# Kernel tuning notes

Measured on AMD Instinct MI355X. Metric: run time of the kernel, lower is better.

Reference implementation:

```python
import jax, jax.numpy as jnp
import numpy as np
import math

B, T, D, H, E, K = 2, 1024, 1024, 2048, 8, 2
CAP_FRAC = 0.25


def setup_inputs() -> dict:
    key = jax.random.key(0)
    ks = jax.random.split(key, 6)
    s = 0.02  # weight scale (orig uses TruncatedNormal; scale kept sane)
    return {
        "x": jax.random.normal(ks[0], (B, T, D), dtype=jnp.float32),
        "router_w": jax.random.normal(ks[1], (D, E), dtype=jnp.float32) * s,
        "router_b": jax.random.normal(ks[2], (E,), dtype=jnp.float32) * s,
        "w1": jax.random.normal(ks[3], (E, D, H), dtype=jnp.float32) * s,
        "w2": jax.random.normal(ks[4], (E, D, H), dtype=jnp.float32) * s,
        "w3": jax.random.normal(ks[5], (E, H, D), dtype=jnp.float32) * s,
    }


def reference(x, router_w, router_b, w1, w2, w3):
    b, t, d = x.shape
    Bt = b * t
    cap = math.floor(Bt * CAP_FRAC)  # expert capacity C (static)
    x_flat = x.reshape(Bt, d)

    # ---- router: fp32 scores, top-k, softmax over selected experts ----
    scores = x_flat.astype(jnp.float32) @ router_w + router_b  # (Bt, E)
    top_scores, assign = jax.lax.top_k(scores, K)               # (Bt, K)
    gates = jax.nn.softmax(top_scores, axis=-1).astype(x.dtype)

    # ---- capacity-based token->expert assignment via one-hot cumsum ----
    onehot = jax.nn.one_hot(assign, E)                          # (Bt, K, E)
    pos = jnp.cumsum(jnp.cumsum(onehot, axis=0), axis=1).astype(jnp.int32)
    mask = onehot * jnp.less(pos, cap)                          # (Bt, K, E)
    token_mask = jnp.sum(mask, axis=-1)                         # (Bt, K)
    # dispatch tensor: (E, C, Bt)
    choices = jnp.sum(jax.nn.one_hot(pos, cap) * mask[..., None], axis=1)
    choices = choices.transpose(1, 2, 0).astype(jnp.int32)
    e_id = jnp.einsum('tke,e->tk', mask, jnp.arange(E, dtype=mask.dtype)).astype(jnp.int32)
    p_id = jnp.einsum('tke,tke->tk', mask, pos.astype(mask.dtype)).astype(jnp.int32)

    # ---- dispatch ----
    grouped = jnp.einsum('ect,td->ecd', choices.astype(x.dtype), x_flat)  # (E, C, D)

    # ---- grouped expert FFN: gelu(w2(x) * w1(x)) @ w3 ----
    h = jnp.einsum('ecd,edh->ech', grouped, w2) * jnp.einsum('ecd,edh->ech', grouped, w1)
    h = jax.nn.gelu(h)
    eo = jnp.einsum('ech,ehd->ecd', h, w3)                      # (E, C, D)

    # ---- combine ----
    e_id = e_id.reshape(b, t, K)
    p_id = p_id.reshape(b, t, K)
    token_mask = token_mask.reshape(b, t, K)
    gates = gates.reshape(b, t, K)
    out = eo[e_id, p_id]                                        # (b, t, K, D)
    out = jnp.where(token_mask[..., None].astype(bool), out, x[..., None, :])
    return jnp.einsum('btkd,btk->btd', out, gates)
```

## Files before the change

kernel.cpp:

```cpp
#include <hip/hip_runtime.h>
#include <hip/hip_bf16.h>
#include <math.h>

#define BT   2048
#define DD   1024
#define HH   2048
#define EE   8
#define CAP  512

typedef unsigned short u16;
typedef unsigned int   u32;
typedef short bf16x8 __attribute__((ext_vector_type(8)));
typedef float f32x4  __attribute__((ext_vector_type(4)));
typedef u16   u16x4  __attribute__((ext_vector_type(4)));

#define AS1 __attribute__((address_space(1)))
#define AS3 __attribute__((address_space(3)))

__device__ __forceinline__ u16 f2bf(float f) {
    union { float f; u32 u; } v; v.f = f;
    return (u16)((v.u + 0x7fffu + ((v.u >> 16) & 1u)) >> 16);
}
__device__ __forceinline__ float bf2f(u16 b) {
    union { u32 u; float f; } v; v.u = ((u32)b) << 16;
    return v.f;
}
__device__ __forceinline__ u32 pkbf(float lo, float hi) {
    u32 r;
    asm("v_cvt_pk_bf16_f32 %0, %1, %2" : "=v"(r) : "v"(lo), "v"(hi));
    return r;
}

__global__ __launch_bounds__(256) void router_kernel(
    const float* __restrict__ x, const float* __restrict__ rw,
    const float* __restrict__ rb, int2* __restrict__ assign,
    float2* __restrict__ gates)
{
    int t   = blockIdx.x;
    int tid = threadIdx.x;
    const float* xr = x + (size_t)t * DD;

    float p[EE];
    #pragma unroll
    for (int e = 0; e < EE; ++e) p[e] = 0.f;

    for (int d = tid; d < DD; d += 256) {
        float xv = xr[d];
        const float4* wr = (const float4*)(rw + (size_t)d * EE);
        float4 w0 = wr[0], w1 = wr[1];
        p[0] += xv * w0.x; p[1] += xv * w0.y; p[2] += xv * w0.z; p[3] += xv * w0.w;
        p[4] += xv * w1.x; p[5] += xv * w1.y; p[6] += xv * w1.z; p[7] += xv * w1.w;
    }
    #pragma unroll
    for (int off = 32; off; off >>= 1) {
        #pragma unroll
        for (int e = 0; e < EE; ++e) p[e] += __shfl_down(p[e], off);
    }
    __shared__ float red[4][EE];
    int wv = tid >> 6, ln = tid & 63;
    if (ln == 0) {
        #pragma unroll
        for (int e = 0; e < EE; ++e) red[wv][e] = p[e];
    }
    __syncthreads();
    if (tid == 0) {
        float s[EE];
        #pragma unroll
        for (int e = 0; e < EE; ++e)
            s[e] = red[0][e] + red[1][e] + red[2][e] + red[3][e] + rb[e];
        int i0 = 0;
        #pragma unroll
        for (int e = 1; e < EE; ++e) if (s[e] > s[i0]) i0 = e;
        int i1 = -1;
        #pragma unroll
        for (int e = 0; e < EE; ++e) {
            if (e == i0) continue;
            if (i1 < 0 || s[e] > s[i1]) i1 = e;
        }
        float e1 = expf(s[i1] - s[i0]);
        float denom = 1.0f + e1;
        assign[t] = make_int2(i0, i1);
        gates[t]  = make_float2(1.0f / denom, e1 / denom);
    }
}

__global__ __launch_bounds__(64) void scan_kernel(
    const int2* __restrict__ assign, int4* __restrict__ meta,
    int2* __restrict__ slot_tok)
{
    __shared__ int c0[64][EE];
    __shared__ int cA[64][EE];
    int l = threadIdx.x;

    for (int i = l; i < EE * CAP; i += 64) slot_tok[i] = make_int2(-1, -1);
    #pragma unroll
    for (int e = 0; e < EE; ++e) { c0[l][e] = 0; cA[l][e] = 0; }
    __syncthreads();

    const int CH = BT / 64;
    int t0 = l * CH;

    for (int t = t0; t < t0 + CH; ++t) {
        int2 a = assign[t];
        c0[l][a.x]++; cA[l][a.x]++; cA[l][a.y]++;
    }
    __syncthreads();

    #pragma unroll
    for (int e = 0; e < EE; ++e) {
        int v = c0[l][e], inc = v;
        for (int d = 1; d < 64; d <<= 1) { int u = __shfl_up(inc, d); if (l >= d) inc += u; }
        c0[l][e] = inc - v;
        v = cA[l][e]; inc = v;
        for (int d = 1; d < 64; d <<= 1) { int u = __shfl_up(inc, d); if (l >= d) inc += u; }
        cA[l][e] = inc - v;
    }
    __syncthreads();

    for (int t = t0; t < t0 + CH; ++t) {
        int2 a = assign[t];
        int p0 = ++c0[l][a.x];  cA[l][a.x]++;
        int p1 = ++cA[l][a.y];
        int4 m;
        m.x = a.x; m.y = (p0 < CAP) ? p0 : -1;
        m.z = a.y; m.w = (p1 < CAP) ? p1 : -1;
        meta[t] = m;
        int* st = (int*)slot_tok;
        if (p0 < CAP) st[(a.x * CAP + p0) * 2 + 0] = t;
        if (p1 < CAP) st[(a.y * CAP + p1) * 2 + 1] = t;
    }
}

__global__ __launch_bounds__(256) void gather_bf16(
    const float* __restrict__ x, const int2* __restrict__ slot_tok,
    u16* __restrict__ G)
{
    int es = blockIdx.x;
    int d  = threadIdx.x * 4;
    int2 st = slot_tok[es];
    float4 r = make_float4(0.f, 0.f, 0.f, 0.f);
    if (st.x >= 0) r = *(const float4*)(x + (size_t)st.x * DD + d);
    if (st.y >= 0) {
        float4 v = *(const float4*)(x + (size_t)st.y * DD + d);
        r.x += v.x; r.y += v.y; r.z += v.z; r.w += v.w;
    }
    u16x4 o;
    o[0] = f2bf(r.x); o[1] = f2bf(r.y); o[2] = f2bf(r.z); o[3] = f2bf(r.w);
    *(u16x4*)(G + (size_t)es * DD + d) = o;
}


__global__ __launch_bounds__(256, 2) void gemm1_mfma(
    const u16* __restrict__ G, const float* __restrict__ W1,
    const float* __restrict__ W2, u16* __restrict__ H)
{
    __shared__ u16   As [128 * 64];
    __shared__ float B1s[64 * 64];
    __shared__ float B2s[64 * 64];

    const int bid  = blockIdx.x;
    const int e    = bid & 7;
    const int rest = bid >> 3;
    const int m0   = (rest & 3) * 128;
    const int n0   = (rest >> 2) * 64;

    const int tid  = threadIdx.x;
    const int lane = tid & 63;
    const int w    = tid >> 6;
    const int lr = lane & 15, lq = lane >> 4;

    const char* Ab  = (const char*)(G + (size_t)e * CAP * DD + (size_t)m0 * DD);
    const char* W1b = (const char*)(W1 + (size_t)e * DD * HH + n0);
    const char* W2b = (const char*)(W2 + (size_t)e * DD * HH + n0);

    const int srow = lane >> 2;
    const int skb  = ((lane & 3) ^ ((lane >> 3) & 3)) * 16;
    const int brow_i = lane >> 4;

    f32x4 acc1[8] = {};
    f32x4 acc2[8] = {};

    for (int k0 = 0; k0 < DD; k0 += 64) {
        #pragma unroll
        for (int j = 0; j < 4; ++j) {
            const int idx = 4 * w + j;
            const int h = idx >> 3, c = idx & 7;
            const size_t rb = (size_t)(c * 16 + srow) * (DD * 2)
                            + (size_t)k0 * 2 + h * 64 + skb;
            __builtin_amdgcn_global_load_lds((const AS1 void*)(Ab + rb),
                (AS3 void*)((char*)As + idx * 1024), 16, 0, 0);
        }
        #pragma unroll
        for (int i = 0; i < 4; ++i) {
            const int krow = w * 16 + i * 4 + brow_i;
            const int bscc = ((lane & 15) ^ ((5 * (2 * w + (i >> 1))) & 15)) * 16;
            const size_t sb = (size_t)(k0 + krow) * (HH * 4) + bscc;
            __builtin_amdgcn_global_load_lds((const AS1 void*)(W1b + sb),
                (AS3 void*)((char*)B1s + w * 4096 + i * 1024), 16, 0, 0);
            __builtin_amdgcn_global_load_lds((const AS1 void*)(W2b + sb),
                (AS3 void*)((char*)B2s + w * 4096 + i * 1024), 16, 0, 0);
        }
        __syncthreads();
        #pragma unroll
        for (int h = 0; h < 2; ++h) {
            bf16x8 av[8];
            #pragma unroll
            for (int m = 0; m < 8; ++m) {
                const int row = m * 16 + lr;
                const int sl  = (lq ^ ((row >> 1) & 3)) * 16;
                av[m] = *(const bf16x8*)((const char*)As + h * 8192 + row * 64 + sl);
            }
            const int n   = w * 16 + lr;
            const int lqh = h * 4 + lq;
            const int cb  = ((((n >> 2) ^ (5 * lqh)) & 15) << 4) + (n & 3) * 4;
            union { u32 q[4]; bf16x8 v; } u1, u2;
            #pragma unroll
            for (int i = 0; i < 4; ++i) {
                int o = (lqh * 8 + 2 * i) * 256 + cb;
                asm("" : "+v"(o));
                u1.q[i] = pkbf(*(const float*)((const char*)B1s + o),
                               *(const float*)((const char*)B1s + o + 256));
                u2.q[i] = pkbf(*(const float*)((const char*)B2s + o),
                               *(const float*)((const char*)B2s + o + 256));
            }
            const bf16x8 b1 = u1.v, b2 = u2.v;
            #pragma unroll
            for (int m = 0; m < 8; ++m) {
                acc1[m] = __builtin_amdgcn_mfma_f32_16x16x32_bf16(av[m], b1, acc1[m], 0, 0, 0);
                acc2[m] = __builtin_amdgcn_mfma_f32_16x16x32_bf16(av[m], b2, acc2[m], 0, 0, 0);
            }
        }
        __syncthreads();
    }

    u16* He = H + (size_t)e * CAP * HH;
    const float gc0 = 0.7978845608028654f, gc1 = 0.044715f;
    const int cc = n0 + w * 16 + lr;
    #pragma unroll
    for (int m = 0; m < 8; ++m)
        #pragma unroll
        for (int r = 0; r < 4; ++r) {
            const int rr = m0 + m * 16 + lq * 4 + r;
            float hv = acc1[m][r] * acc2[m][r];
            float u  = gc0 * (hv + gc1 * hv * hv * hv);
            float th = 1.f - 2.f / (__expf(2.f * u) + 1.f);
            He[(size_t)rr * HH + cc] = f2bf(0.5f * hv * (1.f + th));
        }
}

__global__ __launch_bounds__(256, 2) void gemm2_mfma(
    const u16* __restrict__ Hin, const float* __restrict__ W3, u16* __restrict__ EO)
{
    __shared__ u16   As[128 * 64];
    __shared__ float Bs[64 * 64];

    const int bid  = blockIdx.x;
    const int e    = bid & 7;
    const int rest = bid >> 3;
    const int m0   = (rest & 3) * 128;
    const int n0   = (rest >> 2) * 64;

    const int tid  = threadIdx.x;
    const int lane = tid & 63;
    const int w    = tid >> 6;
    const int lr = lane & 15, lq = lane >> 4;

    const char* Ab  = (const char*)(Hin + (size_t)e * CAP * HH + (size_t)m0 * HH);
    const char* W3b = (const char*)(W3 + (size_t)e * HH * DD + n0);

    const int srow = lane >> 2;
    const int skb  = ((lane & 3) ^ ((lane >> 3) & 3)) * 16;
    const int brow_i = lane >> 4;

    f32x4 acc[8] = {};

    for (int k0 = 0; k0 < HH; k0 += 64) {
        #pragma unroll
        for (int j = 0; j < 4; ++j) {
            const int idx = 4 * w + j;
            const int h = idx >> 3, c = idx & 7;
            const size_t rb = (size_t)(c * 16 + srow) * (HH * 2)
                            + (size_t)k0 * 2 + h * 64 + skb;
            __builtin_amdgcn_global_load_lds((const AS1 void*)(Ab + rb),
                (AS3 void*)((char*)As + idx * 1024), 16, 0, 0);
        }
        #pragma unroll
        for (int i = 0; i < 4; ++i) {
            const int krow = w * 16 + i * 4 + brow_i;
            const int bscc = ((lane & 15) ^ ((5 * (2 * w + (i >> 1))) & 15)) * 16;
            const size_t sb = (size_t)(k0 + krow) * (DD * 4) + bscc;
            __builtin_amdgcn_global_load_lds((const AS1 void*)(W3b + sb),
                (AS3 void*)((char*)Bs + w * 4096 + i * 1024), 16, 0, 0);
        }
        __syncthreads();
        #pragma unroll
        for (int h = 0; h < 2; ++h) {
            bf16x8 av[8];
            #pragma unroll
            for (int m = 0; m < 8; ++m) {
                const int row = m * 16 + lr;
                const int sl  = (lq ^ ((row >> 1) & 3)) * 16;
                av[m] = *(const bf16x8*)((const char*)As + h * 8192 + row * 64 + sl);
            }
            const int n   = w * 16 + lr;
            const int lqh = h * 4 + lq;
            const int cb  = ((((n >> 2) ^ (5 * lqh)) & 15) << 4) + (n & 3) * 4;
            union { u32 q[4]; bf16x8 v; } u3;
            #pragma unroll
            for (int i = 0; i < 4; ++i) {
                int o = (lqh * 8 + 2 * i) * 256 + cb;
                asm("" : "+v"(o));
                u3.q[i] = pkbf(*(const float*)((const char*)Bs + o),
                               *(const float*)((const char*)Bs + o + 256));
            }
            const bf16x8 b3 = u3.v;
            #pragma unroll
            for (int m = 0; m < 8; ++m)
                acc[m] = __builtin_amdgcn_mfma_f32_16x16x32_bf16(av[m], b3, acc[m], 0, 0, 0);
        }
        __syncthreads();
    }

    u16* Oe = EO + (size_t)e * CAP * DD;
    const int cc = n0 + w * 16 + lr;
    #pragma unroll
    for (int m = 0; m < 8; ++m)
        #pragma unroll
        for (int r = 0; r < 4; ++r) {
            const int rr = m0 + m * 16 + lq * 4 + r;
            Oe[(size_t)rr * DD + cc] = f2bf(acc[m][r]);
        }
}

__global__ __launch_bounds__(256) void combine_kernel(
    const float* __restrict__ x, const u16* __restrict__ EO,
    const int4* __restrict__ meta, const float2* __restrict__ gates,
    float* __restrict__ out)
{
    int t = blockIdx.x;
    int d = threadIdx.x * 4;
    int4  m = meta[t];
    float2 g = gates[t];
    float4 xv = *(const float4*)(x + (size_t)t * DD + d);
    float4 v0 = xv, v1 = xv;
    if (m.y >= 0) {
        u16x4 q = *(const u16x4*)(EO + ((size_t)m.x * CAP + m.y) * DD + d);
        v0 = make_float4(bf2f(q[0]), bf2f(q[1]), bf2f(q[2]), bf2f(q[3]));
    }
    if (m.w >= 0) {
        u16x4 q = *(const u16x4*)(EO + ((size_t)m.z * CAP + m.w) * DD + d);
        v1 = make_float4(bf2f(q[0]), bf2f(q[1]), bf2f(q[2]), bf2f(q[3]));
    }
    float4 r;
    r.x = g.x * v0.x + g.y * v1.x;
    r.y = g.x * v0.y + g.y * v1.y;
    r.z = g.x * v0.z + g.y * v1.z;
    r.w = g.x * v0.w + g.y * v1.w;
    *(float4*)(out + (size_t)t * DD + d) = r;
}

extern "C" void kernel_launch(void* const* d_in, const int* in_sizes, int n_in,
                              void* d_out, int out_size, void* d_ws, size_t ws_size,
                              hipStream_t stream)
{
    const float* x  = (const float*)d_in[0];
    const float* rw = (const float*)d_in[1];
    const float* rb = (const float*)d_in[2];
    const float* w1 = (const float*)d_in[3];
    const float* w2 = (const float*)d_in[4];
    const float* w3 = (const float*)d_in[5];
    float* out = (float*)d_out;

    char* ws = (char*)d_ws;
    size_t off = 0;
    auto alloc = [&](size_t bytes) { char* p = ws + off; off = (off + bytes + 255) & ~(size_t)255; return p; };

    int2*   assign   = (int2*)  alloc(BT * sizeof(int2));
    float2* gates    = (float2*)alloc(BT * sizeof(float2));
    int4*   meta     = (int4*)  alloc(BT * sizeof(int4));
    int2*   slot_tok = (int2*)  alloc(EE * CAP * sizeof(int2));
    u16*    grouped  = (u16*)   alloc((size_t)EE * CAP * DD * 2);
    u16*    Hbuf     = (u16*)   alloc((size_t)EE * CAP * HH * 2);
    u16*    eo       = (u16*)   alloc((size_t)EE * CAP * DD * 2);
    (void)ws_size;

    router_kernel<<<BT, 256, 0, stream>>>(x, rw, rb, assign, gates);
    scan_kernel<<<1, 64, 0, stream>>>(assign, meta, slot_tok);
    gather_bf16<<<EE * CAP, 256, 0, stream>>>(x, slot_tok, grouped);

    gemm1_mfma<<<1024, 256, 0, stream>>>(grouped, w1, w2, Hbuf);
    gemm2_mfma<<<512, 256, 0, stream>>>(Hbuf, w3, eo);

    combine_kernel<<<BT, 256, 0, stream>>>(x, eo, meta, gates, out);
}
```

Measured before the change: 128.4 us.

## Split fused dual-weight GEMM1 into two single-weight GEMMs plus elementwise mul-GELU kernel

The fused gemm1 kernel, which computed both w1 and w2 projections and applied the mul-GELU epilogue, becomes a single-weight GEMM launched twice. Each launch writes fp32 results to new workspace buffers, and a separate elementwise kernel multiplies them, applies GELU and writes bf16. This lowers per-block register and LDS pressure, which may help occupancy. The cost is rereading the A tiles twice and a large fp32 round trip through global memory (two 32 MB writes plus reads), along with extra launches.

```diff
diff --git a/kernel.cpp b/kernel.cpp
--- a/kernel.cpp
+++ b/kernel.cpp
@@ -150,13 +150,11 @@
 }
 
 
-__global__ __launch_bounds__(256, 2) void gemm1_mfma(
-    const u16* __restrict__ G, const float* __restrict__ W1,
-    const float* __restrict__ W2, u16* __restrict__ H)
-{
-    __shared__ u16   As [128 * 64];
-    __shared__ float B1s[64 * 64];
-    __shared__ float B2s[64 * 64];
+__global__ __launch_bounds__(256, 2) void gemm_half(
+    const u16* __restrict__ G, const float* __restrict__ W, float* __restrict__ C)
+{
+    __shared__ u16   As[128 * 64];
+    __shared__ float Bs[64 * 64];
 
     const int bid  = blockIdx.x;
     const int e    = bid & 7;
@@ -169,16 +167,14 @@
     const int w    = tid >> 6;
     const int lr = lane & 15, lq = lane >> 4;
 
-    const char* Ab  = (const char*)(G + (size_t)e * CAP * DD + (size_t)m0 * DD);
-    const char* W1b = (const char*)(W1 + (size_t)e * DD * HH + n0);
-    const char* W2b = (const char*)(W2 + (size_t)e * DD * HH + n0);
+    const char* Ab = (const char*)(G + (size_t)e * CAP * DD + (size_t)m0 * DD);
+    const char* Wb = (const char*)(W + (size_t)e * DD * HH + n0);
 
     const int srow = lane >> 2;
     const int skb  = ((lane & 3) ^ ((lane >> 3) & 3)) * 16;
     const int brow_i = lane >> 4;
 
-    f32x4 acc1[8] = {};
-    f32x4 acc2[8] = {};
+    f32x4 acc[8] = {};
 
     for (int k0 = 0; k0 < DD; k0 += 64) {
         #pragma unroll
@@ -195,10 +191,8 @@
             const int krow = w * 16 + i * 4 + brow_i;
             const int bscc = ((lane & 15) ^ ((5 * (2 * w + (i >> 1))) & 15)) * 16;
             const size_t sb = (size_t)(k0 + krow) * (HH * 4) + bscc;
-            __builtin_amdgcn_global_load_lds((const AS1 void*)(W1b + sb),
-                (AS3 void*)((char*)B1s + w * 4096 + i * 1024), 16, 0, 0);
-            __builtin_amdgcn_global_load_lds((const AS1 void*)(W2b + sb),
-                (AS3 void*)((char*)B2s + w * 4096 + i * 1024), 16, 0, 0);
+            __builtin_amdgcn_global_load_lds((const AS1 void*)(Wb + sb),
+                (AS3 void*)((char*)Bs + w * 4096 + i * 1024), 16, 0, 0);
         }
         __syncthreads();
         #pragma unroll
@@ -213,39 +207,51 @@
             const int n   = w * 16 + lr;
             const int lqh = h * 4 + lq;
             const int cb  = ((((n >> 2) ^ (5 * lqh)) & 15) << 4) + (n & 3) * 4;
-            union { u32 q[4]; bf16x8 v; } u1, u2;
+            union { u32 q[4]; bf16x8 v; } ub;
             #pragma unroll
             for (int i = 0; i < 4; ++i) {
                 int o = (lqh * 8 + 2 * i) * 256 + cb;
                 asm("" : "+v"(o));
-                u1.q[i] = pkbf(*(const float*)((const char*)B1s + o),
-                               *(const float*)((const char*)B1s + o + 256));
-                u2.q[i] = pkbf(*(const float*)((const char*)B2s + o),
-                               *(const float*)((const char*)B2s + o + 256));
+                ub.q[i] = pkbf(*(const float*)((const char*)Bs + o),
+                               *(const float*)((const char*)Bs + o + 256));
             }
-            const bf16x8 b1 = u1.v, b2 = u2.v;
-            #pragma unroll
-            for (int m = 0; m < 8; ++m) {
-                acc1[m] = __builtin_amdgcn_mfma_f32_16x16x32_bf16(av[m], b1, acc1[m], 0, 0, 0);
-                acc2[m] = __builtin_amdgcn_mfma_f32_16x16x32_bf16(av[m], b2, acc2[m], 0, 0, 0);
-            }
+            const bf16x8 bfr = ub.v;
+            #pragma unroll
+            for (int m = 0; m < 8; ++m)
+                acc[m] = __builtin_amdgcn_mfma_f32_16x16x32_bf16(av[m], bfr, acc[m], 0, 0, 0);
         }
         __syncthreads();
     }
 
-    u16* He = H + (size_t)e * CAP * HH;
-    const float gc0 = 0.7978845608028654f, gc1 = 0.044715f;
+    float* Ce = C + (size_t)e * CAP * HH;
     const int cc = n0 + w * 16 + lr;
     #pragma unroll
     for (int m = 0; m < 8; ++m)
         #pragma unroll
         for (int r = 0; r < 4; ++r) {
             const int rr = m0 + m * 16 + lq * 4 + r;
-            float hv = acc1[m][r] * acc2[m][r];
-            float u  = gc0 * (hv + gc1 * hv * hv * hv);
-            float th = 1.f - 2.f / (__expf(2.f * u) + 1.f);
-            He[(size_t)rr * HH + cc] = f2bf(0.5f * hv * (1.f + th));
-        }
+            Ce[(size_t)rr * HH + cc] = acc[m][r];
+        }
+}
+
+__global__ __launch_bounds__(256) void mulgelu_kernel(
+    const float* __restrict__ H1, const float* __restrict__ H2,
+    u16* __restrict__ H)
+{
+    const size_t i = ((size_t)blockIdx.x * 256 + threadIdx.x) * 4;
+    float4 a = *(const float4*)(H1 + i);
+    float4 b = *(const float4*)(H2 + i);
+    const float gc0 = 0.7978845608028654f, gc1 = 0.044715f;
+    float hv[4] = { a.x * b.x, a.y * b.y, a.z * b.z, a.w * b.w };
+    u16x4 o;
+    #pragma unroll
+    for (int j = 0; j < 4; ++j) {
+        float v  = hv[j];
+        float u  = gc0 * (v + gc1 * v * v * v);
+        float th = 1.f - 2.f / (__expf(2.f * u) + 1.f);
+        o[j] = f2bf(0.5f * v * (1.f + th));
+    }
+    *(u16x4*)(H + i) = o;
 }
 
 __global__ __launch_bounds__(256, 2) void gemm2_mfma(
@@ -382,13 +388,18 @@
     u16*    grouped  = (u16*)   alloc((size_t)EE * CAP * DD * 2);
     u16*    Hbuf     = (u16*)   alloc((size_t)EE * CAP * HH * 2);
     u16*    eo       = (u16*)   alloc((size_t)EE * CAP * DD * 2);
+    float*  H1buf    = (float*) alloc((size_t)EE * CAP * HH * 4);
+    float*  H2buf    = (float*) alloc((size_t)EE * CAP * HH * 4);
     (void)ws_size;
 
     router_kernel<<<BT, 256, 0, stream>>>(x, rw, rb, assign, gates);
     scan_kernel<<<1, 64, 0, stream>>>(assign, meta, slot_tok);
     gather_bf16<<<EE * CAP, 256, 0, stream>>>(x, slot_tok, grouped);
 
-    gemm1_mfma<<<1024, 256, 0, stream>>>(grouped, w1, w2, Hbuf);
+    gemm_half<<<1024, 256, 0, stream>>>(grouped, w1, H1buf);
+    gemm_half<<<1024, 256, 0, stream>>>(grouped, w2, H2buf);
+    mulgelu_kernel<<<(EE * CAP * HH) / 1024, 256, 0, stream>>>(H1buf, H2buf, Hbuf);
+
     gemm2_mfma<<<512, 256, 0, stream>>>(Hbuf, w3, eo);
 
     combine_kernel<<<BT, 256, 0, stream>>>(x, eo, meta, gates, out);
```

Result: slower. 192.3 us (+49.8%).
